# Optimization experiments

Measured on AMD Instinct MI355X. Metric: run time of the kernel, lower is better.

The kernel has to match this reference:

```python
import jax, jax.numpy as jnp
import numpy as np

STRIDE = 1
PADDING = 1

def setup_inputs() -> dict:
    key = jax.random.key(0)
    k1, k2 = jax.random.split(key)
    x = jax.random.normal(k1, (32, 128, 56, 56), dtype=jnp.float32)
    weight = jax.random.normal(k2, (256, 128, 3, 3), dtype=jnp.float32) * 0.01
    bias = jnp.zeros((256,), dtype=jnp.float32)
    return {"x": x, "weight": weight, "bias": bias}

def reference(x, weight, bias):
    # Same math as unfold (im2col) + matmul conv: a standard 2D cross-correlation.
    # Expressed as lax.conv_general_dilated, the efficient implicit-GEMM form.
    out = jax.lax.conv_general_dilated(
        x, weight,
        window_strides=(STRIDE, STRIDE),
        padding=[(PADDING, PADDING), (PADDING, PADDING)],
        dimension_numbers=("NCHW", "OIHW", "NCHW"),
    )
    out = out + bias[None, :, None, None]
    return out
```

## Files before the change

kernel.cpp:

```cpp
#include <hip/hip_runtime.h>

typedef int   v4i __attribute__((ext_vector_type(4)));
typedef float v4f __attribute__((ext_vector_type(4)));

#define NB 32
#define CI 128
#define HW 56
#define KOC 256
#define HP 58
#define MTOT (NB*HW*HW)
#define XP_ELEMS (NB*HP*HP*CI)
#define WB_ELEMS (9*KOC*CI)
#define XP_OFF_BYTES ((size_t)1<<20)

__device__ __forceinline__ unsigned short f2bf(float f) {
    unsigned int u = __builtin_bit_cast(unsigned int, f);
    u += 0x7fffu + ((u >> 16) & 1u);
    return (unsigned short)(u >> 16);
}

__global__ void wt_bf16(const float* __restrict__ w, unsigned short* __restrict__ wb) {
    int t = blockIdx.x * 256 + threadIdx.x;
    if (t >= KOC * CI) return;
    const float* src = w + (size_t)t * 9;
    int ko = t >> 7, c = t & 127;
    #pragma unroll
    for (int rs = 0; rs < 9; ++rs)
        wb[(size_t)(rs * KOC + ko) * CI + c] = f2bf(src[rs]);
}

__global__ void pad_nhwc_bf16(const float* __restrict__ x, unsigned short* __restrict__ xp) {
    __shared__ unsigned short tile[HW][136];
    int b = blockIdx.x;
    int n = b / HW, h = b % HW;
    int tid = threadIdx.x;
    const float* xr = x + (size_t)n * CI * HW * HW + (size_t)h * HW;
    for (int idx = tid; idx < CI * HW; idx += 256) {
        int c = idx / HW, w = idx % HW;
        tile[w][c] = f2bf(xr[(size_t)c * (HW * HW) + w]);
    }
    __syncthreads();
    unsigned short* xpr = xp + ((size_t)(n * HP + (h + 1)) * HP + 1) * CI;
    for (int idx = tid; idx < (HW * CI) / 8; idx += 256) {
        int w = idx >> 4, c8 = (idx & 15) * 8;
        *reinterpret_cast<uint4*>(xpr + (size_t)w * CI + c8) =
            *reinterpret_cast<const uint4*>(&tile[w][c8]);
    }
}

__global__ __launch_bounds__(256) void conv_mfma(
    const unsigned short* __restrict__ xp,
    const unsigned short* __restrict__ wb,
    const float* __restrict__ bias,
    float* __restrict__ out)
{
    __shared__ unsigned short sW[128][40];
    __shared__ unsigned short sX[128][40];

    const int tid  = threadIdx.x;
    const int lane = tid & 63;
    const int wid  = tid >> 6;
    const int wko  = wid >> 1, wm = wid & 1;
    const int m0   = blockIdx.x * 128;
    const int ko0  = blockIdx.y * 128;

    const int r0 = tid >> 2;
    const int cp = (tid & 3) * 8;

    int mA = m0 + r0,      mB = m0 + 64 + r0;
    int nA = mA / 3136, tA = mA % 3136, ohA = tA / 56, owA = tA % 56;
    int nB = mB / 3136, tB = mB % 3136, ohB = tB / 56, owB = tB % 56;
    size_t xbaseA = ((size_t)(nA * HP + ohA) * HP + owA) * CI;
    size_t xbaseB = ((size_t)(nB * HP + ohB) * HP + owB) * CI;
    size_t wbaseA = (size_t)(ko0 + r0) * CI + cp;
    size_t wbaseB = (size_t)(ko0 + 64 + r0) * CI + cp;

    v4f acc[4][4];
    const v4f vzero = {0.f, 0.f, 0.f, 0.f};
    #pragma unroll
    for (int a = 0; a < 4; ++a)
        #pragma unroll
        for (int b = 0; b < 4; ++b) acc[a][b] = vzero;

    auto ldg = [&](int it, v4i& w0, v4i& w1, v4i& x0, v4i& x1) {
        int rs = it >> 2;
        int cb = (it & 3) * 32;
        int r = rs / 3, s = rs % 3;
        size_t shift = (size_t)(r * HP + s) * CI + cb + cp;
        const unsigned short* wrow = wb + (size_t)rs * KOC * CI + cb;
        w0 = *reinterpret_cast<const v4i*>(wrow + wbaseA);
        w1 = *reinterpret_cast<const v4i*>(wrow + wbaseB);
        x0 = *reinterpret_cast<const v4i*>(xp + xbaseA + shift);
        x1 = *reinterpret_cast<const v4i*>(xp + xbaseB + shift);
    };

    v4i wv0, wv1, xv0, xv1;
    ldg(0, wv0, wv1, xv0, xv1);

    const int aRow = wko * 64 + (lane & 15);
    const int bRow = wm * 64 + (lane & 15);
    const int kOff = (lane >> 4) * 8;

    for (int it = 0; it < 36; ++it) {
        *reinterpret_cast<v4i*>(&sW[r0][cp])      = wv0;
        *reinterpret_cast<v4i*>(&sW[64 + r0][cp]) = wv1;
        *reinterpret_cast<v4i*>(&sX[r0][cp])      = xv0;
        *reinterpret_cast<v4i*>(&sX[64 + r0][cp]) = xv1;
        __syncthreads();

        int nx = (it + 1 < 36) ? it + 1 : 35;
        v4i wn0, wn1, xn0, xn1;
        ldg(nx, wn0, wn1, xn0, xn1);

        v4i af[4], bf[4];
        #pragma unroll
        for (int a = 0; a < 4; ++a)
            af[a] = *reinterpret_cast<const v4i*>(&sW[aRow + a * 16][kOff]);
        #pragma unroll
        for (int b = 0; b < 4; ++b)
            bf[b] = *reinterpret_cast<const v4i*>(&sX[bRow + b * 16][kOff]);

        #pragma unroll
        for (int a = 0; a < 4; ++a)
            #pragma unroll
            for (int b = 0; b < 4; ++b)
                asm volatile("v_mfma_f32_16x16x32_bf16 %0, %1, %2, %0"
                             : "+v"(acc[a][b]) : "v"(af[a]), "v"(bf[b]));

        __syncthreads();
        wv0 = wn0; wv1 = wn1; xv0 = xn0; xv1 = xn1;
    }

    asm volatile("s_nop 7\n\ts_nop 7\n\ts_nop 7"
        : "+v"(acc[0][0]), "+v"(acc[0][1]), "+v"(acc[0][2]), "+v"(acc[0][3]),
          "+v"(acc[1][0]), "+v"(acc[1][1]), "+v"(acc[1][2]), "+v"(acc[1][3]),
          "+v"(acc[2][0]), "+v"(acc[2][1]), "+v"(acc[2][2]), "+v"(acc[2][3]),
          "+v"(acc[3][0]), "+v"(acc[3][1]), "+v"(acc[3][2]), "+v"(acc[3][3]));

    const int koBase = ko0 + wko * 64 + (lane >> 4) * 4;
    float bv[4][4];
    #pragma unroll
    for (int a = 0; a < 4; ++a)
        #pragma unroll
        for (int r = 0; r < 4; ++r)
            bv[a][r] = bias[koBase + a * 16 + r];

    #pragma unroll
    for (int b = 0; b < 4; ++b) {
        int mcol = m0 + wm * 64 + b * 16 + (lane & 15);
        int n = mcol / 3136, t4 = mcol % 3136, oh = t4 / 56, ow = t4 % 56;
        size_t obase = (size_t)n * (KOC * 3136) + (size_t)oh * 56 + ow;
        #pragma unroll
        for (int a = 0; a < 4; ++a) {
            int kk = koBase + a * 16;
            #pragma unroll
            for (int r = 0; r < 4; ++r)
                out[obase + (size_t)(kk + r) * 3136] = acc[a][b][r] + bv[a][r];
        }
    }
}

__global__ void conv_naive(const float* __restrict__ x, const float* __restrict__ w,
                           const float* __restrict__ bias, float* __restrict__ out) {
    int idx = blockIdx.x * 256 + threadIdx.x;
    if (idx >= NB * KOC * HW * HW) return;
    int ow = idx % 56, t = idx / 56, oh = t % 56, t2 = t / 56, ko = t2 % 256, n = t2 / 256;
    float accv = bias[ko];
    for (int c = 0; c < CI; ++c)
        for (int r = 0; r < 3; ++r) {
            int ih = oh - 1 + r;
            if (ih < 0 || ih >= HW) continue;
            for (int s = 0; s < 3; ++s) {
                int iw = ow - 1 + s;
                if (iw < 0 || iw >= HW) continue;
                accv += x[((size_t)(n * CI + c) * HW + ih) * HW + iw] *
                        w[((size_t)(ko * CI + c) * 3 + r) * 3 + s];
            }
        }
    out[idx] = accv;
}

extern "C" void kernel_launch(void* const* d_in, const int* in_sizes, int n_in,
                              void* d_out, int out_size, void* d_ws, size_t ws_size,
                              hipStream_t stream) {
    const float* x    = (const float*)d_in[0];
    const float* w    = (const float*)d_in[1];
    const float* bias = (const float*)d_in[2];
    float* out = (float*)d_out;

    size_t need = XP_OFF_BYTES + (size_t)XP_ELEMS * 2;
    if (ws_size < need) {
        int tot = NB * KOC * HW * HW;
        conv_naive<<<dim3((tot + 255) / 256), dim3(256), 0, stream>>>(x, w, bias, out);
        return;
    }

    unsigned short* wbp = (unsigned short*)d_ws;
    unsigned short* xpd = (unsigned short*)((char*)d_ws + XP_OFF_BYTES);

    hipMemsetAsync(xpd, 0, (size_t)XP_ELEMS * 2, stream);
    wt_bf16<<<dim3((KOC * CI + 255) / 256), dim3(256), 0, stream>>>(w, wbp);
    pad_nhwc_bf16<<<dim3(NB * HW), dim3(256), 0, stream>>>(x, xpd);

    dim3 grid(MTOT / 128, 2);
    conv_mfma<<<grid, dim3(256), 0, stream>>>(xpd, wbp, bias, out);
}
```

Baseline: 123.8 us.

## Double-buffer conv tiles via direct global-to-LDS loads with XOR swizzle

Restructures the MFMA conv main loop to load tiles straight from global memory into LDS with global_load_lds, double-buffered, using a K-step of 64 instead of 32 so there are 18 iterations with one barrier each. LDS rows are XOR-swizzled to avoid bank conflicts, and MFMA blocks are wrapped with s_setprio. The full-buffer memset is replaced by a kernel that zeroes only the padding border. The larger LDS footprint (64KB) may limit occupancy despite the launch_bounds hint, and the direct-to-LDS load path adds ordering requirements.

```diff
diff --git a/kernel.cpp b/kernel.cpp
--- a/kernel.cpp
+++ b/kernel.cpp
@@ -2,6 +2,7 @@
 
 typedef int   v4i __attribute__((ext_vector_type(4)));
 typedef float v4f __attribute__((ext_vector_type(4)));
+typedef unsigned short ushort_t;
 
 #define NB 32
 #define CI 128
@@ -9,8 +10,7 @@
 #define KOC 256
 #define HP 58
 #define MTOT (NB*HW*HW)
-#define XP_ELEMS (NB*HP*HP*CI)
-#define WB_ELEMS (9*KOC*CI)
+#define XP_ELEMS ((size_t)NB*HP*HP*CI)
 #define XP_OFF_BYTES ((size_t)1<<20)
 
 __device__ __forceinline__ unsigned short f2bf(float f) {
@@ -19,7 +19,13 @@
     return (unsigned short)(u >> 16);
 }
 
-__global__ void wt_bf16(const float* __restrict__ w, unsigned short* __restrict__ wb) {
+__device__ __forceinline__ void gload16(const void* g, void* l) {
+    __builtin_amdgcn_global_load_lds(
+        (const __attribute__((address_space(1))) void*)g,
+        (__attribute__((address_space(3))) void*)l, 16, 0, 0);
+}
+
+__global__ void wt_bf16(const float* __restrict__ w, ushort_t* __restrict__ wb) {
     int t = blockIdx.x * 256 + threadIdx.x;
     if (t >= KOC * CI) return;
     const float* src = w + (size_t)t * 9;
@@ -29,8 +35,8 @@
         wb[(size_t)(rs * KOC + ko) * CI + c] = f2bf(src[rs]);
 }
 
-__global__ void pad_nhwc_bf16(const float* __restrict__ x, unsigned short* __restrict__ xp) {
-    __shared__ unsigned short tile[HW][136];
+__global__ void pad_nhwc_bf16(const float* __restrict__ x, ushort_t* __restrict__ xp) {
+    __shared__ ushort_t tile[HW][136];
     int b = blockIdx.x;
     int n = b / HW, h = b % HW;
     int tid = threadIdx.x;
@@ -40,7 +46,7 @@
         tile[w][c] = f2bf(xr[(size_t)c * (HW * HW) + w]);
     }
     __syncthreads();
-    unsigned short* xpr = xp + ((size_t)(n * HP + (h + 1)) * HP + 1) * CI;
+    ushort_t* xpr = xp + ((size_t)(n * HP + (h + 1)) * HP + 1) * CI;
     for (int idx = tid; idx < (HW * CI) / 8; idx += 256) {
         int w = idx >> 4, c8 = (idx & 15) * 8;
         *reinterpret_cast<uint4*>(xpr + (size_t)w * CI + c8) =
@@ -48,32 +54,62 @@
     }
 }
 
-__global__ __launch_bounds__(256) void conv_mfma(
-    const unsigned short* __restrict__ xp,
-    const unsigned short* __restrict__ wb,
+__global__ void border_zero(ushort_t* __restrict__ xp) {
+    int t = blockIdx.x * 256 + threadIdx.x;
+    if (t >= NB * 228 * 16) return;
+    int c16 = t & 15;
+    int p = (t >> 4) % 228;
+    int n = t / (228 * 16);
+    int h, wc;
+    if (p < 58)       { h = 0;               wc = p; }
+    else if (p < 116) { h = 57;              wc = p - 58; }
+    else { int q = p - 116; h = 1 + (q >> 1); wc = (q & 1) * 57; }
+    size_t off = ((size_t)(n * HP + h) * HP + wc) * CI + (size_t)c16 * 8;
+    uint4 z; z.x = z.y = z.z = z.w = 0u;
+    *reinterpret_cast<uint4*>(xp + off) = z;
+}
+
+__global__ __launch_bounds__(256, 2) void conv_mfma(
+    const ushort_t* __restrict__ xp,
+    const ushort_t* __restrict__ wb,
     const float* __restrict__ bias,
     float* __restrict__ out)
 {
-    __shared__ unsigned short sW[128][40];
-    __shared__ unsigned short sX[128][40];
+    __shared__ alignas(16) ushort_t sW[2][128 * 64];
+    __shared__ alignas(16) ushort_t sX[2][128 * 64];
 
     const int tid  = threadIdx.x;
     const int lane = tid & 63;
-    const int wid  = tid >> 6;
-    const int wko  = wid >> 1, wm = wid & 1;
+    const int wv   = tid >> 6;
+    const int wko  = wv >> 1, wm = wv & 1;
     const int m0   = blockIdx.x * 128;
     const int ko0  = blockIdx.y * 128;
 
-    const int r0 = tid >> 2;
-    const int cp = (tid & 3) * 8;
-
-    int mA = m0 + r0,      mB = m0 + 64 + r0;
-    int nA = mA / 3136, tA = mA % 3136, ohA = tA / 56, owA = tA % 56;
-    int nB = mB / 3136, tB = mB % 3136, ohB = tB / 56, owB = tB % 56;
-    size_t xbaseA = ((size_t)(nA * HP + ohA) * HP + owA) * CI;
-    size_t xbaseB = ((size_t)(nB * HP + ohB) * HP + owB) * CI;
-    size_t wbaseA = (size_t)(ko0 + r0) * CI + cp;
-    size_t wbaseB = (size_t)(ko0 + 64 + r0) * CI + cp;
+    const int srow   = lane >> 3;
+    const int schunk = (lane & 7) ^ srow;
+    const ushort_t* wsrc[4];
+    const ushort_t* xsrc[4];
+    #pragma unroll
+    for (int j = 0; j < 4; ++j) {
+        int row = wv * 32 + j * 8 + srow;
+        wsrc[j] = wb + (size_t)(ko0 + row) * CI + schunk * 8;
+        int m = m0 + row;
+        int n = m / 3136, tt = m % 3136, oh = tt / 56, ow = tt % 56;
+        xsrc[j] = xp + ((size_t)(n * HP + oh) * HP + ow) * CI + schunk * 8;
+    }
+
+    const int lm = lane & 15, lk = lane >> 4, l7 = lane & 7;
+    int offA[4][2], offB[4][2];
+    #pragma unroll
+    for (int a = 0; a < 4; ++a)
+        #pragma unroll
+        for (int h = 0; h < 2; ++h) {
+            int rowA = wko * 64 + a * 16 + lm;
+            int rowB = wm  * 64 + a * 16 + lm;
+            int s = (h * 4 + lk) ^ l7;
+            offA[a][h] = rowA * 64 + s * 8;
+            offB[a][h] = rowB * 64 + s * 8;
+        }
 
     v4f acc[4][4];
     const v4f vzero = {0.f, 0.f, 0.f, 0.f};
@@ -82,53 +118,50 @@
         #pragma unroll
         for (int b = 0; b < 4; ++b) acc[a][b] = vzero;
 
-    auto ldg = [&](int it, v4i& w0, v4i& w1, v4i& x0, v4i& x1) {
-        int rs = it >> 2;
-        int cb = (it & 3) * 32;
-        int r = rs / 3, s = rs % 3;
-        size_t shift = (size_t)(r * HP + s) * CI + cb + cp;
-        const unsigned short* wrow = wb + (size_t)rs * KOC * CI + cb;
-        w0 = *reinterpret_cast<const v4i*>(wrow + wbaseA);
-        w1 = *reinterpret_cast<const v4i*>(wrow + wbaseB);
-        x0 = *reinterpret_cast<const v4i*>(xp + xbaseA + shift);
-        x1 = *reinterpret_cast<const v4i*>(xp + xbaseB + shift);
+    auto stage = [&](int buf, int t) {
+        int rs = t >> 1;
+        int r  = (rs * 11) >> 5;
+        int s  = rs - r * 3;
+        int ch = (t & 1) << 6;
+        int woff = rs * (KOC * CI) + ch;
+        int xoff = (r * HP + s) * CI + ch;
+        char* dW = (char*)&sW[0][0] + buf * 16384 + wv * 4096;
+        char* dX = (char*)&sX[0][0] + buf * 16384 + wv * 4096;
+        #pragma unroll
+        for (int j = 0; j < 4; ++j) {
+            gload16(wsrc[j] + woff, dW + j * 1024);
+            gload16(xsrc[j] + xoff, dX + j * 1024);
+        }
     };
 
-    v4i wv0, wv1, xv0, xv1;
-    ldg(0, wv0, wv1, xv0, xv1);
-
-    const int aRow = wko * 64 + (lane & 15);
-    const int bRow = wm * 64 + (lane & 15);
-    const int kOff = (lane >> 4) * 8;
-
-    for (int it = 0; it < 36; ++it) {
-        *reinterpret_cast<v4i*>(&sW[r0][cp])      = wv0;
-        *reinterpret_cast<v4i*>(&sW[64 + r0][cp]) = wv1;
-        *reinterpret_cast<v4i*>(&sX[r0][cp])      = xv0;
-        *reinterpret_cast<v4i*>(&sX[64 + r0][cp]) = xv1;
+    stage(0, 0);
+    __syncthreads();
+
+    for (int t = 0; t < 18; ++t) {
+        int cur = t & 1;
+        if (t < 17) stage(cur ^ 1, t + 1);
+
+        const ushort_t* bW = &sW[cur][0];
+        const ushort_t* bX = &sX[cur][0];
+        #pragma unroll
+        for (int h = 0; h < 2; ++h) {
+            v4i af[4], bf[4];
+            #pragma unroll
+            for (int a = 0; a < 4; ++a)
+                af[a] = *reinterpret_cast<const v4i*>(bW + offA[a][h]);
+            #pragma unroll
+            for (int b = 0; b < 4; ++b)
+                bf[b] = *reinterpret_cast<const v4i*>(bX + offB[b][h]);
+            __builtin_amdgcn_s_setprio(1);
+            #pragma unroll
+            for (int a = 0; a < 4; ++a)
+                #pragma unroll
+                for (int b = 0; b < 4; ++b)
+                    asm volatile("v_mfma_f32_16x16x32_bf16 %0, %1, %2, %0"
+                                 : "+v"(acc[a][b]) : "v"(af[a]), "v"(bf[b]));
+            __builtin_amdgcn_s_setprio(0);
+        }
         __syncthreads();
-
-        int nx = (it + 1 < 36) ? it + 1 : 35;
-        v4i wn0, wn1, xn0, xn1;
-        ldg(nx, wn0, wn1, xn0, xn1);
-
-        v4i af[4], bf[4];
-        #pragma unroll
-        for (int a = 0; a < 4; ++a)
-            af[a] = *reinterpret_cast<const v4i*>(&sW[aRow + a * 16][kOff]);
-        #pragma unroll
-        for (int b = 0; b < 4; ++b)
-            bf[b] = *reinterpret_cast<const v4i*>(&sX[bRow + b * 16][kOff]);
-
-        #pragma unroll
-        for (int a = 0; a < 4; ++a)
-            #pragma unroll
-            for (int b = 0; b < 4; ++b)
-                asm volatile("v_mfma_f32_16x16x32_bf16 %0, %1, %2, %0"
-                             : "+v"(acc[a][b]) : "v"(af[a]), "v"(bf[b]));
-
-        __syncthreads();
-        wv0 = wn0; wv1 = wn1; xv0 = xn0; xv1 = xn1;
     }
 
     asm volatile("s_nop 7\n\ts_nop 7\n\ts_nop 7"
@@ -188,17 +221,17 @@
     const float* bias = (const float*)d_in[2];
     float* out = (float*)d_out;
 
-    size_t need = XP_OFF_BYTES + (size_t)XP_ELEMS * 2;
+    size_t need = XP_OFF_BYTES + XP_ELEMS * 2;
     if (ws_size < need) {
         int tot = NB * KOC * HW * HW;
         conv_naive<<<dim3((tot + 255) / 256), dim3(256), 0, stream>>>(x, w, bias, out);
         return;
     }
 
-    unsigned short* wbp = (unsigned short*)d_ws;
-    unsigned short* xpd = (unsigned short*)((char*)d_ws + XP_OFF_BYTES);
-
-    hipMemsetAsync(xpd, 0, (size_t)XP_ELEMS * 2, stream);
+    ushort_t* wbp = (ushort_t*)d_ws;
+    ushort_t* xpd = (ushort_t*)((char*)d_ws + XP_OFF_BYTES);
+
+    border_zero<<<dim3((NB * 228 * 16 + 255) / 256), dim3(256), 0, stream>>>(xpd);
     wt_bf16<<<dim3((KOC * CI + 255) / 256), dim3(256), 0, stream>>>(w, wbp);
     pad_nhwc_bf16<<<dim3(NB * HW), dim3(256), 0, stream>>>(x, xpd);
 
```

Measured after the change: 115.4 us. 6.8% less time.
